# Kernel tuning notes

Hardware: AMD Instinct MI355X
Metric: run time of the kernel (lower is better)

## Reference

```python
import math
import jax, jax.numpy as jnp
import numpy as np

S = 30.0
M = 0.5
COS_M = math.cos(M)
SIN_M = math.sin(M)
THRESHOLD = math.cos(math.pi - M)
MM = math.sin(math.pi - M) * M


def setup_inputs() -> dict:
    key = jax.random.key(0)
    k1, k2, k3 = jax.random.split(key, 3)
    B, D, C = 512, 512, 100000
    return {
        "embeddings": jax.random.normal(k1, (B, D), dtype=jnp.float32),
        "kernel": jax.random.normal(k2, (D, C), dtype=jnp.float32) * 0.01,
        "label": jax.random.randint(k3, (B,), 0, C),
        "t": jnp.zeros((1,), dtype=jnp.float32),
    }


def reference(embeddings, kernel, label, t):
    B = embeddings.shape[0]
    # dual L2 normalization (rows of embeddings, columns of kernel)
    emb = embeddings / jnp.linalg.norm(embeddings, ord=2, axis=1, keepdims=True)
    kn = kernel / jnp.linalg.norm(kernel, ord=2, axis=0, keepdims=True)
    # [B, C] cosine similarity, clamped
    cosine = jnp.clip(emb @ kn, -1.0, 1.0)
    rows = jnp.arange(B)
    target_logit = cosine[rows, label][:, None]  # [B, 1]
    sin_theta = jnp.sqrt(1.0 - target_logit ** 2)
    cos_theta_m = target_logit * COS_M - sin_theta * SIN_M  # cos(theta + m)
    # hard negatives: cosine > cos(theta_y + m)
    mask = cosine > cos_theta_m
    final_target = jnp.where(target_logit > THRESHOLD, cos_theta_m, target_logit - MM)
    # EMA update of t (no-grad in the original)
    t_new = target_logit.mean() * 0.01 + 0.99 * t  # shape (1,)
    # scale hard negatives by (t + cosine), fused predicated write
    scaled = jnp.where(mask, cosine * (t_new[0] + cosine), cosine)
    # scatter target logit back into its column
    out = scaled.at[rows, label].set(final_target[:, 0])
    return out * S
```

## Files before the change

### kernel.cpp

```cpp
#include <hip/hip_runtime.h>

#define CC 100000
#define DD 512

#define S_SCALE 30.0f
#define COS_M_C 0.8775825618903728f
#define SIN_M_C 0.479425538604203f
#define THRESH_C (-0.8775825618903728f)
#define MM_C 0.2397127693021015f

typedef __attribute__((ext_vector_type(8))) short short8;
typedef __attribute__((ext_vector_type(4))) float f32x4;

static __device__ __forceinline__ unsigned short f2bf(float x) {
  unsigned int u = __float_as_uint(x);
  unsigned int r = (u + 0x7fffu + ((u >> 16) & 1u)) >> 16;
  return (unsigned short)r;
}

#define FENCE() __builtin_amdgcn_sched_barrier(0)

__global__ __launch_bounds__(64) void k1_prep(
    const float* __restrict__ emb, const float* __restrict__ kern,
    const int* __restrict__ label, unsigned short* __restrict__ wsA,
    float* __restrict__ ws_target, float* __restrict__ ws_ctm,
    float* __restrict__ ws_ft) {
  const int i = blockIdx.x;
  const int l = threadIdx.x;

  const float4* er = reinterpret_cast<const float4*>(emb + (size_t)i * DD + l * 8);
  float4 v0 = er[0], v1 = er[1];
  float e[8] = {v0.x, v0.y, v0.z, v0.w, v1.x, v1.y, v1.z, v1.w};

  float esq = 0.f;
#pragma unroll
  for (int j = 0; j < 8; ++j) esq += e[j] * e[j];
#pragma unroll
  for (int o = 32; o > 0; o >>= 1) esq += __shfl_xor(esq, o);
  const float inv = rsqrtf(esq);

  const int c = label[i];
  float dot = 0.f, wsq = 0.f;
#pragma unroll
  for (int j = 0; j < 8; ++j) {
    float w = kern[(size_t)(l * 8 + j) * CC + c];
    dot += e[j] * w;
    wsq += w * w;
  }
#pragma unroll
  for (int o = 32; o > 0; o >>= 1) {
    dot += __shfl_xor(dot, o);
    wsq += __shfl_xor(wsq, o);
  }

  unsigned int pk[4];
#pragma unroll
  for (int j = 0; j < 4; ++j) {
    unsigned int lo = f2bf(e[2 * j] * inv);
    unsigned int hi = f2bf(e[2 * j + 1] * inv);
    pk[j] = lo | (hi << 16);
  }
  const int kb = l >> 2;
  const int off = kb * 32768 + i * 64 + ((16 * (l & 3)) ^ ((i & 3) << 4));
  uint4 v; v.x = pk[0]; v.y = pk[1]; v.z = pk[2]; v.w = pk[3];
  *reinterpret_cast<uint4*>(reinterpret_cast<char*>(wsA) + off) = v;

  if (l == 0) {
    float t = dot * rsqrtf(fmaxf(esq * wsq, 1e-30f));
    t = fminf(fmaxf(t, -1.f), 1.f);
    float st = sqrtf(fmaxf(0.f, 1.f - t * t));
    float ctm = t * COS_M_C - st * SIN_M_C;
    ws_target[i] = t;
    ws_ctm[i] = ctm;
    ws_ft[i] = (t > THRESH_C) ? ctm : (t - MM_C);
  }
}

__global__ __launch_bounds__(64) void k2_tnew(const float* __restrict__ ws_target,
                                              const float* __restrict__ t_in,
                                              float* __restrict__ ws_tnew) {
  const int l = threadIdx.x;
  float s = 0.f;
#pragma unroll
  for (int j = 0; j < 8; ++j) s += ws_target[l * 8 + j];
#pragma unroll
  for (int o = 32; o > 0; o >>= 1) s += __shfl_xor(s, o);
  if (l == 0) ws_tnew[0] = 0.01f * (s * (1.0f / 512.0f)) + 0.99f * t_in[0];
}

__global__ __launch_bounds__(512, 4) void k3_gemm(
    const float* __restrict__ kern, const unsigned short* __restrict__ wsA,
    const int* __restrict__ label, const float* __restrict__ ws_ctm,
    const float* __restrict__ ws_ft, const float* __restrict__ ws_tnew,
    float* __restrict__ out) {
  __shared__ __align__(16) unsigned short Alds[2][512 * 32];
  __shared__ __align__(16) unsigned short Blds[2][64 * 32];
  __shared__ float colsq[64];

  const int t = threadIdx.x;
  const int l = t & 63;
  const int wv = t >> 6;
  const int n0 = blockIdx.x * 64;

  if (t < 64) colsq[t] = 0.f;

  const int bn = l;
  const int gcol = n0 + bn;
  const bool colok = gcol < CC;
  const float* bcol = kern + gcol;

  float sumsq = 0.f;

  f32x4 acc[4][4];
#pragma unroll
  for (int a = 0; a < 4; ++a)
#pragma unroll
    for (int b = 0; b < 4; ++b) acc[a][b] = (f32x4){0.f, 0.f, 0.f, 0.f};

  const int lr = l & 15;
  const int lg = l >> 4;
  const int swz = (lg * 16) ^ ((lr & 3) << 4);
  char* Ab = reinterpret_cast<char*>(Alds);
  char* Bb = reinterpret_cast<char*>(Blds);

#define BLOAD(KT, r0, r1, r2, r3)                                        \
  {                                                                      \
    if (colok) {                                                         \
      const float* p_ = bcol + (size_t)((KT) * 32 + wv * 4) * CC;        \
      r0 = p_[0];                                                        \
      r1 = p_[(size_t)CC];                                               \
      r2 = p_[(size_t)2 * CC];                                           \
      r3 = p_[(size_t)3 * CC];                                           \
    } else {                                                             \
      r0 = r1 = r2 = r3 = 0.f;                                           \
    }                                                                    \
  }

#define AGLL(KT)                                                         \
  {                                                                      \
    const char* gA_ = reinterpret_cast<const char*>(wsA) + (KT) * 32768; \
    char* lA_ = Ab + ((KT)&1) * 32768;                                   \
    _Pragma("unroll") for (int i_ = 0; i_ < 4; ++i_) {                   \
      const int o_ = i_ * 8192 + t * 16;                                 \
      __builtin_amdgcn_global_load_lds(                                  \
          (const __attribute__((address_space(1))) unsigned int*)(gA_ + o_), \
          (__attribute__((address_space(3))) unsigned int*)(lA_ + o_),   \
          16, 0, 0);                                                     \
    }                                                                    \
  }

#define BWRITE(KT, r0, r1, r2, r3)                                       \
  {                                                                      \
    sumsq += r0 * r0 + r1 * r1 + r2 * r2 + r3 * r3;                      \
    uint2 pk_;                                                           \
    pk_.x = (unsigned int)f2bf(r0) | ((unsigned int)f2bf(r1) << 16);     \
    pk_.y = (unsigned int)f2bf(r2) | ((unsigned int)f2bf(r3) << 16);     \
    *reinterpret_cast<uint2*>(Bb + ((KT)&1) * 4096 + bn * 64 +           \
                              ((wv * 8) ^ ((bn & 3) << 4))) = pk_;       \
  }

  float c0, c1, c2, c3;
  float p0, p1, p2, p3;
  BLOAD(0, c0, c1, c2, c3);
  FENCE();
  AGLL(0);
  FENCE();
  BLOAD(1, p0, p1, p2, p3);
  FENCE();
  AGLL(1);
  FENCE();
  BWRITE(0, c0, c1, c2, c3);
  FENCE();
  asm volatile("s_waitcnt vmcnt(8)" ::: "memory");
  asm volatile("s_waitcnt lgkmcnt(0)" ::: "memory");
  FENCE();
  __builtin_amdgcn_s_barrier();
  FENCE();

  for (int kt = 0; kt < 16; ++kt) {
    const int cur = kt & 1;
    short8 af[4], bfr[4];
#pragma unroll
    for (int mf = 0; mf < 4; ++mf) {
      const int m = wv * 64 + mf * 16 + lr;
      af[mf] = *reinterpret_cast<const short8*>(Ab + cur * 32768 + m * 64 + swz);
    }
#pragma unroll
    for (int nf = 0; nf < 4; ++nf) {
      const int n = nf * 16 + lr;
      bfr[nf] = *reinterpret_cast<const short8*>(Bb + cur * 4096 + n * 64 + swz);
    }
    if (kt < 15) {
      asm volatile("s_waitcnt vmcnt(4)" ::: "memory");
      BWRITE(kt + 1, p0, p1, p2, p3);
    }
    __builtin_amdgcn_s_setprio(1);
#pragma unroll
    for (int mf = 0; mf < 4; ++mf)
#pragma unroll
      for (int nf = 0; nf < 4; ++nf)
        acc[mf][nf] = __builtin_amdgcn_mfma_f32_16x16x32_bf16(
            af[mf], bfr[nf], acc[mf][nf], 0, 0, 0);
    __builtin_amdgcn_s_setprio(0);
    asm volatile("s_waitcnt lgkmcnt(0)" ::: "memory");
    FENCE();
    __builtin_amdgcn_s_barrier();
    FENCE();
    if (kt < 14) {
      BLOAD(kt + 2, p0, p1, p2, p3);
      FENCE();
      AGLL(kt + 2);
      FENCE();
      asm volatile("s_waitcnt vmcnt(8)" ::: "memory");
    } else {
      asm volatile("s_waitcnt vmcnt(0)" ::: "memory");
    }
    FENCE();
    __builtin_amdgcn_s_barrier();
    FENCE();
  }

  atomicAdd(&colsq[bn], sumsq);
  asm volatile("s_waitcnt lgkmcnt(0)" ::: "memory");
  FENCE();
  __builtin_amdgcn_s_barrier();
  FENCE();

  const float tnew = ws_tnew[0];
  float invn[4];
#pragma unroll
  for (int nf = 0; nf < 4; ++nf)
    invn[nf] = rsqrtf(fmaxf(colsq[nf * 16 + lr], 1e-30f));

  float* est = reinterpret_cast<float*>(Alds) + (size_t)wv * 1088;
  const int c4 = n0 + lr * 4;
#pragma unroll
  for (int mf = 0; mf < 4; ++mf) {
    asm volatile("s_waitcnt lgkmcnt(0)" ::: "memory");
    FENCE();
#pragma unroll
    for (int r = 0; r < 4; ++r)
#pragma unroll
      for (int nf = 0; nf < 4; ++nf)
        est[(lg * 4 + r) * 68 + nf * 16 + lr] = acc[mf][nf][r] * invn[nf];
    asm volatile("s_waitcnt lgkmcnt(0)" ::: "memory");
    FENCE();
#pragma unroll
    for (int p = 0; p < 4; ++p) {
      const int rr = p * 4 + lg;
      const int m = wv * 64 + mf * 16 + rr;
      const float ctm = ws_ctm[m];
      const float ft = ws_ft[m];
      const int lab = label[m];
      float4 vv = *reinterpret_cast<const float4*>(&est[rr * 68 + lr * 4]);
      if (c4 < CC) {
        float ov[4] = {vv.x, vv.y, vv.z, vv.w};
#pragma unroll
        for (int j = 0; j < 4; ++j) {
          float cosv = fminf(fmaxf(ov[j], -1.f), 1.f);
          float val = (cosv > ctm) ? cosv * (tnew + cosv) : cosv;
          if (c4 + j == lab) val = ft;
          ov[j] = val * S_SCALE;
        }
        float4 st4;
        st4.x = ov[0]; st4.y = ov[1]; st4.z = ov[2]; st4.w = ov[3];
        *reinterpret_cast<float4*>(out + (size_t)m * CC + c4) = st4;
      }
    }
  }
#undef BLOAD
#undef AGLL
#undef BWRITE
}

extern "C" void kernel_launch(void* const* d_in, const int* in_sizes, int n_in,
                              void* d_out, int out_size, void* d_ws,
                              size_t ws_size, hipStream_t stream) {
  (void)in_sizes; (void)n_in; (void)out_size; (void)ws_size;
  const float* emb = (const float*)d_in[0];
  const float* kern = (const float*)d_in[1];
  const int* label = (const int*)d_in[2];
  const float* t_in = (const float*)d_in[3];
  float* out = (float*)d_out;

  char* ws = (char*)d_ws;
  unsigned short* wsA = (unsigned short*)ws;
  float* ws_target = (float*)(ws + 524288);
  float* ws_ctm = (float*)(ws + 526336);
  float* ws_ft = (float*)(ws + 528384);
  float* ws_tnew = (float*)(ws + 530432);

  k1_prep<<<512, 64, 0, stream>>>(emb, kern, label, wsA, ws_target, ws_ctm, ws_ft);
  k2_tnew<<<1, 64, 0, stream>>>(ws_target, t_in, ws_tnew);
  k3_gemm<<<(CC + 63) / 64, 512, 0, stream>>>(kern, wsA, label, ws_ctm, ws_ft,
                                              ws_tnew, out);
}
```

Baseline: 153.7 us.

## Deepen B-tile register prefetch to three stages and fully unroll K loop

The B tile global loads now run one more K-step ahead, using a two-slot register queue, so the wait before each B write to LDS no longer stalls on a just-issued load. The K loop is fully unrolled through a macro so queue slot indices and the vmcnt thresholds are compile-time constants. The cost is more live registers and larger code, and a wrong vmcnt count could read stale data.

```diff
diff --git a/kernel.cpp b/kernel.cpp
--- a/kernel.cpp
+++ b/kernel.cpp
@@ -159,16 +159,20 @@
                               ((wv * 8) ^ ((bn & 3) << 4))) = pk_;       \
   }
 
+  float bq[2][4];
+
   float c0, c1, c2, c3;
-  float p0, p1, p2, p3;
   BLOAD(0, c0, c1, c2, c3);
   FENCE();
   AGLL(0);
   FENCE();
-  BLOAD(1, p0, p1, p2, p3);
+  BLOAD(1, bq[1][0], bq[1][1], bq[1][2], bq[1][3]);
   FENCE();
   AGLL(1);
   FENCE();
+  BLOAD(2, bq[0][0], bq[0][1], bq[0][2], bq[0][3]);
+  FENCE();
+  asm volatile("s_waitcnt vmcnt(16)" ::: "memory");
   BWRITE(0, c0, c1, c2, c3);
   FENCE();
   asm volatile("s_waitcnt vmcnt(8)" ::: "memory");
@@ -177,48 +181,59 @@
   __builtin_amdgcn_s_barrier();
   FENCE();
 
-  for (int kt = 0; kt < 16; ++kt) {
-    const int cur = kt & 1;
-    short8 af[4], bfr[4];
-#pragma unroll
-    for (int mf = 0; mf < 4; ++mf) {
-      const int m = wv * 64 + mf * 16 + lr;
-      af[mf] = *reinterpret_cast<const short8*>(Ab + cur * 32768 + m * 64 + swz);
-    }
-#pragma unroll
-    for (int nf = 0; nf < 4; ++nf) {
-      const int n = nf * 16 + lr;
-      bfr[nf] = *reinterpret_cast<const short8*>(Bb + cur * 4096 + n * 64 + swz);
-    }
-    if (kt < 15) {
-      asm volatile("s_waitcnt vmcnt(4)" ::: "memory");
-      BWRITE(kt + 1, p0, p1, p2, p3);
-    }
-    __builtin_amdgcn_s_setprio(1);
-#pragma unroll
-    for (int mf = 0; mf < 4; ++mf)
-#pragma unroll
-      for (int nf = 0; nf < 4; ++nf)
-        acc[mf][nf] = __builtin_amdgcn_mfma_f32_16x16x32_bf16(
-            af[mf], bfr[nf], acc[mf][nf], 0, 0, 0);
-    __builtin_amdgcn_s_setprio(0);
-    asm volatile("s_waitcnt lgkmcnt(0)" ::: "memory");
-    FENCE();
-    __builtin_amdgcn_s_barrier();
-    FENCE();
-    if (kt < 14) {
-      BLOAD(kt + 2, p0, p1, p2, p3);
-      FENCE();
-      AGLL(kt + 2);
-      FENCE();
-      asm volatile("s_waitcnt vmcnt(8)" ::: "memory");
-    } else {
-      asm volatile("s_waitcnt vmcnt(0)" ::: "memory");
-    }
-    FENCE();
-    __builtin_amdgcn_s_barrier();
-    FENCE();
-  }
+#define KBODY(KT)                                                          \
+  {                                                                        \
+    constexpr int cur_ = (KT)&1;                                           \
+    constexpr int ws_ = ((KT) + 1) & 1;                                    \
+    short8 af[4], bfr[4];                                                  \
+    _Pragma("unroll") for (int mf = 0; mf < 4; ++mf) {                     \
+      const int m = wv * 64 + mf * 16 + lr;                                \
+      af[mf] =                                                             \
+          *reinterpret_cast<const short8*>(Ab + cur_ * 32768 + m * 64 + swz); \
+    }                                                                      \
+    _Pragma("unroll") for (int nf = 0; nf < 4; ++nf) {                     \
+      const int n = nf * 16 + lr;                                          \
+      bfr[nf] =                                                            \
+          *reinterpret_cast<const short8*>(Bb + cur_ * 4096 + n * 64 + swz);  \
+    }                                                                      \
+    if ((KT) < 15) {                                                       \
+      BWRITE((KT) + 1, bq[ws_][0], bq[ws_][1], bq[ws_][2], bq[ws_][3]);    \
+    }                                                                      \
+    __builtin_amdgcn_s_setprio(1);                                         \
+    _Pragma("unroll") for (int mf = 0; mf < 4; ++mf)                       \
+        _Pragma("unroll") for (int nf = 0; nf < 4; ++nf) acc[mf][nf] =     \
+        __builtin_amdgcn_mfma_f32_16x16x32_bf16(af[mf], bfr[nf],           \
+                                                acc[mf][nf], 0, 0, 0);     \
+    __builtin_amdgcn_s_setprio(0);                                         \
+    asm volatile("s_waitcnt lgkmcnt(0)" ::: "memory");                     \
+    FENCE();                                                               \
+    __builtin_amdgcn_s_barrier();                                          \
+    FENCE();                                                               \
+    if ((KT) < 13) {                                                       \
+      BLOAD((KT) + 3, bq[ws_][0], bq[ws_][1], bq[ws_][2], bq[ws_][3]);     \
+      FENCE();                                                             \
+    }                                                                      \
+    if ((KT) < 14) {                                                       \
+      AGLL((KT) + 2);                                                      \
+      FENCE();                                                             \
+    }                                                                      \
+    if ((KT) < 13) {                                                       \
+      asm volatile("s_waitcnt vmcnt(8)" ::: "memory");                     \
+    } else if ((KT) == 13) {                                               \
+      asm volatile("s_waitcnt vmcnt(4)" ::: "memory");                     \
+    } else {                                                               \
+      asm volatile("s_waitcnt vmcnt(0)" ::: "memory");                     \
+    }                                                                      \
+    FENCE();                                                               \
+    __builtin_amdgcn_s_barrier();                                          \
+    FENCE();                                                               \
+  }
+
+  KBODY(0) KBODY(1) KBODY(2) KBODY(3) KBODY(4) KBODY(5) KBODY(6) KBODY(7)
+  KBODY(8) KBODY(9) KBODY(10) KBODY(11) KBODY(12) KBODY(13) KBODY(14)
+  KBODY(15)
+
+#undef KBODY
 
   atomicAdd(&colsq[bn], sumsq);
   asm volatile("s_waitcnt lgkmcnt(0)" ::: "memory");
```

Measured after the change: 395.8 us. 2.57x slower.

## Load A fragments directly from global in MFMA layout, drop A LDS staging

Applied to the files above, without the earlier changes.

The prep kernel now writes the normalized bf16 embeddings in a fragment-ordered layout, so each wave can load its A operands straight from global/L2 into registers instead of staging the full 512x32 A tile through LDS with global_load_lds. The K loop is restructured into 8 steps of 64, with 8 B rows loaded per thread, XOR-swizzled 128-byte B rows, and a single barrier per step instead of two. This shrinks LDS use to about 34 KB and halves the barrier count, aiming for higher occupancy and less synchronization. In exchange, every wave reads A from global memory, which raises L2 traffic and exposes more load latency inside the loop.

```diff
diff --git a/kernel.cpp b/kernel.cpp
--- a/kernel.cpp
+++ b/kernel.cpp
@@ -60,8 +60,8 @@
     unsigned int hi = f2bf(e[2 * j + 1] * inv);
     pk[j] = lo | (hi << 16);
   }
-  const int kb = l >> 2;
-  const int off = kb * 32768 + i * 64 + ((16 * (l & 3)) ^ ((i & 3) << 4));
+  const int off = (l >> 2) * 32768 + (i >> 6) * 4096 + (((i >> 4) & 3)) * 1024 +
+                  ((l & 3) * 16 + (i & 15)) * 16;
   uint4 v; v.x = pk[0]; v.y = pk[1]; v.z = pk[2]; v.w = pk[3];
   *reinterpret_cast<uint4*>(reinterpret_cast<char*>(wsA) + off) = v;
 
@@ -93,8 +93,7 @@
     const int* __restrict__ label, const float* __restrict__ ws_ctm,
     const float* __restrict__ ws_ft, const float* __restrict__ ws_tnew,
     float* __restrict__ out) {
-  __shared__ __align__(16) unsigned short Alds[2][512 * 32];
-  __shared__ __align__(16) unsigned short Blds[2][64 * 32];
+  __shared__ __align__(16) char smem[34816];
   __shared__ float colsq[64];
 
   const int t = threadIdx.x;
@@ -109,115 +108,108 @@
   const bool colok = gcol < CC;
   const float* bcol = kern + gcol;
 
-  float sumsq = 0.f;
-
-  f32x4 acc[4][4];
-#pragma unroll
-  for (int a = 0; a < 4; ++a)
-#pragma unroll
-    for (int b = 0; b < 4; ++b) acc[a][b] = (f32x4){0.f, 0.f, 0.f, 0.f};
-
   const int lr = l & 15;
   const int lg = l >> 4;
-  const int swz = (lg * 16) ^ ((lr & 3) << 4);
-  char* Ab = reinterpret_cast<char*>(Alds);
-  char* Bb = reinterpret_cast<char*>(Blds);
-
-#define BLOAD(KT, r0, r1, r2, r3)                                        \
+
+  float sumsq = 0.f;
+
+  f32x4 acc[4][4];
+#pragma unroll
+  for (int a = 0; a < 4; ++a)
+#pragma unroll
+    for (int b = 0; b < 4; ++b) acc[a][b] = (f32x4){0.f, 0.f, 0.f, 0.f};
+
+  char* Bb = smem;
+  const char* pA0 = reinterpret_cast<const char*>(wsA) + wv * 4096 + l * 16;
+  const int rdsw0 = lr * 128 + ((lg ^ (lr & 7)) << 4);
+  const int rdsw1 = lr * 128 + (((4 + lg) ^ (lr & 7)) << 4);
+  const int wroff = bn * 128 + ((wv ^ (bn & 7)) << 4);
+
+  float p0, p1, p2, p3, p4, p5, p6, p7;
+  short8 afA[4], afB[4];
+
+#define BLOAD8(KB)                                                       \
   {                                                                      \
     if (colok) {                                                         \
-      const float* p_ = bcol + (size_t)((KT) * 32 + wv * 4) * CC;        \
-      r0 = p_[0];                                                        \
-      r1 = p_[(size_t)CC];                                               \
-      r2 = p_[(size_t)2 * CC];                                           \
-      r3 = p_[(size_t)3 * CC];                                           \
+      const float* q_ = bcol + (size_t)(KB) * CC;                        \
+      p0 = q_[0];              p1 = q_[(size_t)CC];                      \
+      p2 = q_[(size_t)2 * CC]; p3 = q_[(size_t)3 * CC];                  \
+      p4 = q_[(size_t)4 * CC]; p5 = q_[(size_t)5 * CC];                  \
+      p6 = q_[(size_t)6 * CC]; p7 = q_[(size_t)7 * CC];                  \
     } else {                                                             \
-      r0 = r1 = r2 = r3 = 0.f;                                           \
+      p0 = p1 = p2 = p3 = p4 = p5 = p6 = p7 = 0.f;                       \
     }                                                                    \
   }
 
-#define AGLL(KT)                                                         \
+#define BWRITE8(G1)                                                      \
   {                                                                      \
-    const char* gA_ = reinterpret_cast<const char*>(wsA) + (KT) * 32768; \
-    char* lA_ = Ab + ((KT)&1) * 32768;                                   \
-    _Pragma("unroll") for (int i_ = 0; i_ < 4; ++i_) {                   \
-      const int o_ = i_ * 8192 + t * 16;                                 \
-      __builtin_amdgcn_global_load_lds(                                  \
-          (const __attribute__((address_space(1))) unsigned int*)(gA_ + o_), \
-          (__attribute__((address_space(3))) unsigned int*)(lA_ + o_),   \
-          16, 0, 0);                                                     \
+    sumsq += p0 * p0 + p1 * p1 + p2 * p2 + p3 * p3 + p4 * p4 + p5 * p5 + \
+             p6 * p6 + p7 * p7;                                          \
+    uint4 pk_;                                                           \
+    pk_.x = (unsigned int)f2bf(p0) | ((unsigned int)f2bf(p1) << 16);     \
+    pk_.y = (unsigned int)f2bf(p2) | ((unsigned int)f2bf(p3) << 16);     \
+    pk_.z = (unsigned int)f2bf(p4) | ((unsigned int)f2bf(p5) << 16);     \
+    pk_.w = (unsigned int)f2bf(p6) | ((unsigned int)f2bf(p7) << 16);     \
+    *reinterpret_cast<uint4*>(Bb + ((G1)&1) * 8192 + wroff) = pk_;       \
+  }
+
+#define ALOAD(DST, BYTEOFF)                                              \
+  _Pragma("unroll") for (int mf_ = 0; mf_ < 4; ++mf_) DST[mf_] =         \
+      *reinterpret_cast<const short8*>(pA0 + (BYTEOFF) + mf_ * 1024);
+
+#define MFMA16(AF, BSEL, RDSW)                                           \
+  {                                                                      \
+    short8 bfr0 =                                                        \
+        *reinterpret_cast<const short8*>(Bb + (BSEL) + 0 * 2048 + (RDSW)); \
+    short8 bfr1 =                                                        \
+        *reinterpret_cast<const short8*>(Bb + (BSEL) + 1 * 2048 + (RDSW)); \
+    _Pragma("unroll") for (int mf_ = 0; mf_ < 4; ++mf_) {                \
+      acc[mf_][0] = __builtin_amdgcn_mfma_f32_16x16x32_bf16(             \
+          AF[mf_], bfr0, acc[mf_][0], 0, 0, 0);                          \
+      acc[mf_][1] = __builtin_amdgcn_mfma_f32_16x16x32_bf16(             \
+          AF[mf_], bfr1, acc[mf_][1], 0, 0, 0);                          \
     }                                                                    \
-  }
-
-#define BWRITE(KT, r0, r1, r2, r3)                                       \
-  {                                                                      \
-    sumsq += r0 * r0 + r1 * r1 + r2 * r2 + r3 * r3;                      \
-    uint2 pk_;                                                           \
-    pk_.x = (unsigned int)f2bf(r0) | ((unsigned int)f2bf(r1) << 16);     \
-    pk_.y = (unsigned int)f2bf(r2) | ((unsigned int)f2bf(r3) << 16);     \
-    *reinterpret_cast<uint2*>(Bb + ((KT)&1) * 4096 + bn * 64 +           \
-                              ((wv * 8) ^ ((bn & 3) << 4))) = pk_;       \
-  }
-
-  float c0, c1, c2, c3;
-  float p0, p1, p2, p3;
-  BLOAD(0, c0, c1, c2, c3);
-  FENCE();
-  AGLL(0);
-  FENCE();
-  BLOAD(1, p0, p1, p2, p3);
-  FENCE();
-  AGLL(1);
-  FENCE();
-  BWRITE(0, c0, c1, c2, c3);
-  FENCE();
-  asm volatile("s_waitcnt vmcnt(8)" ::: "memory");
+    short8 bfr2 =                                                        \
+        *reinterpret_cast<const short8*>(Bb + (BSEL) + 2 * 2048 + (RDSW)); \
+    short8 bfr3 =                                                        \
+        *reinterpret_cast<const short8*>(Bb + (BSEL) + 3 * 2048 + (RDSW)); \
+    _Pragma("unroll") for (int mf_ = 0; mf_ < 4; ++mf_) {                \
+      acc[mf_][2] = __builtin_amdgcn_mfma_f32_16x16x32_bf16(             \
+          AF[mf_], bfr2, acc[mf_][2], 0, 0, 0);                          \
+      acc[mf_][3] = __builtin_amdgcn_mfma_f32_16x16x32_bf16(             \
+          AF[mf_], bfr3, acc[mf_][3], 0, 0, 0);                          \
+    }                                                                    \
+  }
+
+  BLOAD8(wv * 8);
+  FENCE();
+  ALOAD(afA, 0);
+  FENCE();
+  BWRITE8(0);
   asm volatile("s_waitcnt lgkmcnt(0)" ::: "memory");
   FENCE();
   __builtin_amdgcn_s_barrier();
   FENCE();
 
-  for (int kt = 0; kt < 16; ++kt) {
-    const int cur = kt & 1;
-    short8 af[4], bfr[4];
-#pragma unroll
-    for (int mf = 0; mf < 4; ++mf) {
-      const int m = wv * 64 + mf * 16 + lr;
-      af[mf] = *reinterpret_cast<const short8*>(Ab + cur * 32768 + m * 64 + swz);
-    }
-#pragma unroll
-    for (int nf = 0; nf < 4; ++nf) {
-      const int n = nf * 16 + lr;
-      bfr[nf] = *reinterpret_cast<const short8*>(Bb + cur * 4096 + n * 64 + swz);
-    }
-    if (kt < 15) {
-      asm volatile("s_waitcnt vmcnt(4)" ::: "memory");
-      BWRITE(kt + 1, p0, p1, p2, p3);
-    }
+  for (int g = 0; g < 8; ++g) {
+    const int bsel = (g & 1) * 8192;
+    ALOAD(afB, g * 65536 + 32768);
+    if (g < 7) { BLOAD8(64 * (g + 1) + wv * 8); }
+    FENCE();
     __builtin_amdgcn_s_setprio(1);
-#pragma unroll
-    for (int mf = 0; mf < 4; ++mf)
-#pragma unroll
-      for (int nf = 0; nf < 4; ++nf)
-        acc[mf][nf] = __builtin_amdgcn_mfma_f32_16x16x32_bf16(
-            af[mf], bfr[nf], acc[mf][nf], 0, 0, 0);
+    MFMA16(afA, bsel, rdsw0);
+    __builtin_amdgcn_s_setprio(0);
+    FENCE();
+    if (g < 7) { ALOAD(afA, (g + 1) * 65536); }
+    FENCE();
+    if (g < 7) { BWRITE8(g + 1); }
+    __builtin_amdgcn_s_setprio(1);
+    MFMA16(afB, bsel, rdsw1);
     __builtin_amdgcn_s_setprio(0);
     asm volatile("s_waitcnt lgkmcnt(0)" ::: "memory");
     FENCE();
     __builtin_amdgcn_s_barrier();
     FENCE();
-    if (kt < 14) {
-      BLOAD(kt + 2, p0, p1, p2, p3);
-      FENCE();
-      AGLL(kt + 2);
-      FENCE();
-      asm volatile("s_waitcnt vmcnt(8)" ::: "memory");
-    } else {
-      asm volatile("s_waitcnt vmcnt(0)" ::: "memory");
-    }
-    FENCE();
-    __builtin_amdgcn_s_barrier();
-    FENCE();
   }
 
   atomicAdd(&colsq[bn], sumsq);
@@ -232,7 +224,7 @@
   for (int nf = 0; nf < 4; ++nf)
     invn[nf] = rsqrtf(fmaxf(colsq[nf * 16 + lr], 1e-30f));
 
-  float* est = reinterpret_cast<float*>(Alds) + (size_t)wv * 1088;
+  float* est = reinterpret_cast<float*>(smem) + (size_t)wv * 1088;
   const int c4 = n0 + lr * 4;
 #pragma unroll
   for (int mf = 0; mf < 4; ++mf) {
@@ -268,9 +260,10 @@
       }
     }
   }
-#undef BLOAD
-#undef AGLL
-#undef BWRITE
+#undef BLOAD8
+#undef BWRITE8
+#undef ALOAD
+#undef MFMA16
 }
 
 extern "C" void kernel_launch(void* const* d_in, const int* in_sizes, int n_in,
```

Measured after the change: 388.5 us. +152.8%, slower.
